# Kernel optimization log

Hardware: AMD Instinct MI355X
Metric: run time of the kernel (lower is better)

The kernel has to match this reference:

```python
import jax, jax.numpy as jnp
import numpy as np

B, T, S, D, H, DH = 2, 2048, 2048, 1024, 16, 64
LN_EPS = 1e-5


def setup_inputs() -> dict:
    key = jax.random.key(0)
    ks = jax.random.split(key, 8)
    return {
        "x": jax.random.normal(ks[0], (B, T, D), jnp.float32),
        "context": jax.random.normal(ks[1], (B, S, D), jnp.float32),
        "lookup_table": jax.random.normal(ks[2], (2 * T - 1, DH), jnp.float32),
        "Wq": jax.random.normal(ks[3], (D, H * DH), jnp.float32) * 0.02,
        "Wk": jax.random.normal(ks[4], (D, H * DH), jnp.float32) * 0.02,
        "Wv": jax.random.normal(ks[5], (D, H * DH), jnp.float32) * 0.02,
        "Wo": jax.random.normal(ks[6], (H * DH, D), jnp.float32) * 0.02,
        "bo": jnp.zeros((D,), jnp.float32),
        "gamma": jnp.ones((D,), jnp.float32),
        "beta": jnp.zeros((D,), jnp.float32),
    }


def skew(QE):
    # QE: [B, H, T, 2T-1] -> [B, H, T, T] via pad/reshape relative-position trick
    b, h, t, _ = QE.shape
    QE = jnp.pad(QE, ((0, 0), (0, 0), (0, 0), (0, 1))).reshape(b, h, -1)
    QE = jnp.pad(QE, ((0, 0), (0, 0), (0, t - 1))).reshape(b, h, t + 1, 2 * t - 1)
    return QE[:, :, :t, -t:]


def reference(x, context, lookup_table, Wq, Wk, Wv, Wo, bo, gamma, beta):
    scale = 1.0 / jnp.sqrt(jnp.asarray(DH, x.dtype))
    # pre-layernorm on queries
    mu = jnp.mean(x, axis=-1, keepdims=True)
    var = jnp.var(x, axis=-1, keepdims=True)
    xn = (x - mu) / jnp.sqrt(var + LN_EPS) * gamma + beta
    q = (xn @ Wq).reshape(B, T, H, DH).transpose(0, 2, 1, 3)       # [B,H,T,DH]
    k = (context @ Wk).reshape(B, S, H, DH).transpose(0, 2, 1, 3)  # [B,H,S,DH]
    v = (context @ Wv).reshape(B, S, H, DH).transpose(0, 2, 1, 3)  # [B,H,S,DH]
    score = jnp.einsum("bhtd,bhsd->bhts", q, k) * scale            # [B,H,T,S]
    rel = skew(jnp.einsum("bhtd,ld->bhtl", q, lookup_table))       # [B,H,T,T]
    # NOTE: faithful to original — QK^T gets scaled twice, rel term once
    score = (score + rel) * scale
    attn = jax.nn.softmax(score, axis=-1)
    out = jnp.einsum("bhts,bhsd->bhtd", attn, v)
    out = out.transpose(0, 2, 1, 3).reshape(B, T, H * DH)
    out = out @ Wo + bo
    # dropout=0 (eval); residual uses the layernormed x (as in source)
    return xn + out
```

## Files before the change

### kernel.cpp

```cpp
#include <hip/hip_runtime.h>

#define DEVFN __device__ __forceinline__

typedef __bf16 bf16x8 __attribute__((ext_vector_type(8)));
typedef float f32x4 __attribute__((ext_vector_type(4)));
typedef unsigned short u16;


DEVFN u16 f2bf(float f) {
  unsigned u = __builtin_bit_cast(unsigned, f);
  u += 0x7FFFu + ((u >> 16) & 1u);
  return (u16)(u >> 16);
}

DEVFN f32x4 mfma16(bf16x8 a, bf16x8 b, f32x4 c) {
  return __builtin_amdgcn_mfma_f32_16x16x32_bf16(a, b, c, 0, 0, 0);
}

DEVFN void gl16(const u16* g, u16* l) {
  __builtin_amdgcn_global_load_lds(
      (const __attribute__((address_space(1))) unsigned int*)g,
      (__attribute__((address_space(3))) unsigned int*)l, 16, 0, 0);
}

__global__ __launch_bounds__(256) void ln_kernel(const float* __restrict__ x,
                                                 const float* __restrict__ gamma,
                                                 const float* __restrict__ beta,
                                                 float* __restrict__ xn,
                                                 u16* __restrict__ xnb) {
  int row = blockIdx.x;
  int tid = threadIdx.x;
  const float4* xr = (const float4*)(x + (size_t)row * 1024);
  float4 v = xr[tid];
  float s = v.x + v.y + v.z + v.w;
  float q = v.x * v.x + v.y * v.y + v.z * v.z + v.w * v.w;
#pragma unroll
  for (int m = 1; m < 64; m <<= 1) {
    s += __shfl_xor(s, m);
    q += __shfl_xor(q, m);
  }
  __shared__ float rs[4], rq[4];
  int w = tid >> 6;
  if ((tid & 63) == 0) { rs[w] = s; rq[w] = q; }
  __syncthreads();
  s = rs[0] + rs[1] + rs[2] + rs[3];
  q = rq[0] + rq[1] + rq[2] + rq[3];
  float mean = s * (1.0f / 1024.0f);
  float var = q * (1.0f / 1024.0f) - mean * mean;
  float inv = rsqrtf(var + 1e-5f);
  float4 g = ((const float4*)gamma)[tid];
  float4 bt = ((const float4*)beta)[tid];
  float4 o;
  o.x = (v.x - mean) * inv * g.x + bt.x;
  o.y = (v.y - mean) * inv * g.y + bt.y;
  o.z = (v.z - mean) * inv * g.z + bt.z;
  o.w = (v.w - mean) * inv * g.w + bt.w;
  ((float4*)(xn + (size_t)row * 1024))[tid] = o;
  ushort4 ob;
  ob.x = f2bf(o.x); ob.y = f2bf(o.y); ob.z = f2bf(o.z); ob.w = f2bf(o.w);
  ((ushort4*)(xnb + (size_t)row * 1024))[tid] = ob;
}

__global__ __launch_bounds__(256) void cvt2_kernel(const float* __restrict__ a,
                                                   u16* __restrict__ oa,
                                                   const float* __restrict__ bsrc,
                                                   u16* __restrict__ ob) {
  int blk = blockIdx.x;
  if (blk < 4096) {
    int i = blk * 256 + threadIdx.x;
    float4 v = ((const float4*)a)[i];
    ushort4 o;
    o.x = f2bf(v.x); o.y = f2bf(v.y); o.z = f2bf(v.z); o.w = f2bf(v.w);
    ((ushort4*)oa)[i] = o;
  } else {
    int i = (blk - 4096) * 256 + threadIdx.x;
    if (i < 65520) {
      float4 v = ((const float4*)bsrc)[i];
      ushort4 o;
      o.x = f2bf(v.x); o.y = f2bf(v.y); o.z = f2bf(v.z); o.w = f2bf(v.w);
      ((ushort4*)ob)[i] = o;
    }
  }
}

__global__ __launch_bounds__(256) void transW_kernel(const float* __restrict__ W0,
                                                     const float* __restrict__ W1,
                                                     const float* __restrict__ W2,
                                                     const float* __restrict__ W3,
                                                     u16* __restrict__ Wall) {
  __shared__ float tile[32][33];
  int z = blockIdx.z;
  const float* W = (z == 0) ? W0 : (z == 1) ? W1 : (z == 2) ? W2 : W3;
  float scale = (z == 0) ? 0.18033688011112042f : (z == 1) ? 0.125f : 1.0f;
  u16* Wt = Wall + (size_t)z * 1048576;
  int tx = threadIdx.x, ty = threadIdx.y;
  int x = blockIdx.x * 32 + tx;
  int y0 = blockIdx.y * 32;
#pragma unroll
  for (int j = 0; j < 32; j += 8)
    tile[ty + j][tx] = W[(size_t)(y0 + ty + j) * 1024 + x];
  __syncthreads();
#pragma unroll
  for (int j = 0; j < 32; j += 8)
    Wt[(size_t)(blockIdx.x * 32 + ty + j) * 1024 + y0 + tx] = f2bf(tile[tx][ty + j] * scale);
}

DEVFN void gemm_core(const u16* __restrict__ A, const u16* __restrict__ Bt,
                     u16* Ab, u16* Bb, int row0, int n0, int tid,
                     f32x4 (&acc)[2][4]) {
  int lane = tid & 63, wv = tid >> 6;
  int l16 = lane & 15, lhi = lane >> 4;
  int r8 = lane >> 3, c8 = lane & 7;
  int cx = ((c8 ^ r8) << 3);
  int swz = (l16 & 7) << 3;

  auto stage = [&](int k0) {
#pragma unroll
    for (int i = 0; i < 4; ++i) {
      int rowb = wv * 32 + i * 8;
      gl16(&A[(size_t)(row0 + rowb + r8) * 1024 + k0 + cx], &Ab[rowb * 64]);
    }
#pragma unroll
    for (int i = 0; i < 2; ++i) {
      int rowb = wv * 16 + i * 8;
      gl16(&Bt[(size_t)(n0 + rowb + r8) * 1024 + k0 + cx], &Bb[rowb * 64]);
    }
  };

  stage(0);
  asm volatile("s_waitcnt vmcnt(0)" ::: "memory");
  __syncthreads();
  for (int kk = 0; kk < 16; ++kk) {
    __builtin_amdgcn_s_setprio(1);
#pragma unroll
    for (int ks = 0; ks < 2; ++ks) {
      bf16x8 af[2], bfr[4];
#pragma unroll
      for (int mi = 0; mi < 2; ++mi) {
        int row = wv * 32 + mi * 16 + l16;
        af[mi] = *(const bf16x8*)&Ab[row * 64 + ((ks * 32 + lhi * 8) ^ swz)];
      }
#pragma unroll
      for (int ni = 0; ni < 4; ++ni) {
        int row = ni * 16 + l16;
        bfr[ni] = *(const bf16x8*)&Bb[row * 64 + ((ks * 32 + lhi * 8) ^ swz)];
      }
#pragma unroll
      for (int mi = 0; mi < 2; ++mi)
#pragma unroll
        for (int ni = 0; ni < 4; ++ni)
          acc[mi][ni] = mfma16(af[mi], bfr[ni], acc[mi][ni]);
    }
    __builtin_amdgcn_s_setprio(0);
    if (kk < 15) {
      __syncthreads();
      stage((kk + 1) * 64);
      asm volatile("s_waitcnt vmcnt(0)" ::: "memory");
      __syncthreads();
    }
  }
}

__global__ __launch_bounds__(256, 4) void qkv_kernel(const u16* __restrict__ xnb,
                                                     const u16* __restrict__ ctxb,
                                                     const u16* __restrict__ Wall,
                                                     u16* __restrict__ qb,
                                                     u16* __restrict__ kb,
                                                     u16* __restrict__ vtb) {
  __shared__ __align__(16) u16 Ab[128 * 64];
  __shared__ __align__(16) u16 Bb[64 * 64];
  int z = blockIdx.z;
  const u16* A = (z == 0) ? xnb : ctxb;
  const u16* Bt = Wall + (size_t)z * 1048576;
  int row0 = blockIdx.x * 128, n0 = blockIdx.y * 64;
  f32x4 acc[2][4] = {};
  gemm_core(A, Bt, Ab, Bb, row0, n0, threadIdx.x, acc);
  int tid = threadIdx.x, lane = tid & 63, wv = tid >> 6;
  int l16 = lane & 15, lhi = lane >> 4;
  u16* qk = (z == 0) ? qb : kb;
#pragma unroll
  for (int mi = 0; mi < 2; ++mi)
#pragma unroll
    for (int ni = 0; ni < 4; ++ni)
#pragma unroll
      for (int r = 0; r < 4; ++r) {
        int m = row0 + wv * 32 + mi * 16 + lhi * 4 + r;
        int n = n0 + ni * 16 + l16;
        int b = m >> 11, t = m & 2047, h = n >> 6, dh = n & 63;
        u16 val = f2bf(acc[mi][ni][r]);
        if (z < 2) {
          qk[(size_t)((b * 16 + h) * 2048 + t) * 64 + dh] = val;
        } else {
          int t2 = (t & ~63) | ((t & 15) << 2) | ((t >> 4) & 3);
          vtb[(size_t)((b * 16 + h) * 64 + dh) * 2048 + t2] = val;
        }
      }
}

__global__ __launch_bounds__(256, 4) void oproj_kernel(const u16* __restrict__ attnb,
                                                       const u16* __restrict__ Wall,
                                                       const float* __restrict__ bias,
                                                       const float* __restrict__ resid,
                                                       float* __restrict__ outF) {
  __shared__ __align__(16) u16 Ab[128 * 64];
  __shared__ __align__(16) u16 Bb[64 * 64];
  const u16* Bt = Wall + (size_t)3 * 1048576;
  int row0 = blockIdx.x * 128, n0 = blockIdx.y * 64;
  f32x4 acc[2][4] = {};
  gemm_core(attnb, Bt, Ab, Bb, row0, n0, threadIdx.x, acc);
  int tid = threadIdx.x, lane = tid & 63, wv = tid >> 6;
  int l16 = lane & 15, lhi = lane >> 4;
#pragma unroll
  for (int mi = 0; mi < 2; ++mi)
#pragma unroll
    for (int ni = 0; ni < 4; ++ni)
#pragma unroll
      for (int r = 0; r < 4; ++r) {
        int m = row0 + wv * 32 + mi * 16 + lhi * 4 + r;
        int n = n0 + ni * 16 + l16;
        outF[(size_t)m * 1024 + n] = acc[mi][ni][r] + bias[n] + resid[(size_t)m * 1024 + n];
      }
}

__global__ __launch_bounds__(256, 4) void flash_kernel(
    const u16* __restrict__ Qg, const u16* __restrict__ Kg,
    const u16* __restrict__ Vtg, const u16* __restrict__ Lb,
    u16* __restrict__ Og) {
  constexpr int T = 2048, H = 16;
  int p = blockIdx.x;
  int bid = (p & 7) * 128 + (p >> 3);
  int qb = bid & 31, h = (bid >> 5) & 15, b = bid >> 9;
  int tid = threadIdx.x;
  int lane = tid & 63, w = tid >> 6;
  int l16 = lane & 15, lhi = lane >> 4;

  __shared__ __align__(16) u16 Klds[64 * 64];
  __shared__ __align__(16) u16 Vt[64 * 64];
  __shared__ __align__(16) u16 Llds[128 * 64];
  __shared__ __align__(16) u16 Plds[4][16 * 64];

  const u16* qbase = Qg + (size_t)(b * H + h) * T * 64;
  const u16* kbase = Kg + (size_t)(b * H + h) * T * 64;
  const u16* vtbase = Vtg + (size_t)(b * H + h) * 64 * 2048;

  int i0b = qb * 64;
  int i0w = i0b + w * 16;
  bf16x8 aq[2];
  aq[0] = *(const bf16x8*)&qbase[(i0w + l16) * 64 + lhi * 8];
  aq[1] = *(const bf16x8*)&qbase[(i0w + l16) * 64 + 32 + lhi * 8];

  f32x4 accO[4] = {};
  float mrun[4], lsum[4];
#pragma unroll
  for (int r = 0; r < 4; ++r) { mrun[r] = -1e30f; lsum[r] = 0.0f; }

  int bandbase = T - 16 - i0w;
  int ubase0 = T - 64 - i0b;
  int uoff = 48 - 16 * w;

  int r8 = lane >> 3, c8 = lane & 7;
  int cx = ((c8 ^ r8) << 3);
  int swz = (l16 & 7) << 3;

  auto stageKL = [&](int j0) {
#pragma unroll
    for (int i = 0; i < 2; ++i) {
      int rowb = w * 16 + i * 8;
      gl16(&kbase[(size_t)(j0 + rowb + r8) * 64 + cx], &Klds[rowb * 64]);
    }
#pragma unroll
    for (int i = 0; i < 4; ++i) {
      int rowb = w * 32 + i * 8;
      gl16(&Lb[(size_t)(ubase0 + j0 + rowb + r8) * 64 + cx], &Llds[rowb * 64]);
    }
  };
  auto stageV = [&](int j0) {
#pragma unroll
    for (int i = 0; i < 2; ++i) {
      int rowb = w * 16 + i * 8;
      gl16(&vtbase[(size_t)(rowb + r8) * 2048 + j0 + cx], &Vt[rowb * 64]);
    }
  };

  const u16* lp = Lb + (size_t)(bandbase + l16) * 64 + lhi * 8;
  f32x4 eC = {};
#pragma unroll
  for (int ks = 0; ks < 2; ++ks)
    eC = mfma16(aq[ks], *(const bf16x8*)&lp[ks * 32], eC);

  f32x4 accS[4];
  f32x4 accE[5];
  auto computeQKE = [&]() {
#pragma unroll
    for (int kb = 0; kb < 4; ++kb) accS[kb] = f32x4{0.f, 0.f, 0.f, 0.f};
    accE[0] = eC;
#pragma unroll
    for (int c = 1; c < 5; ++c) accE[c] = f32x4{0.f, 0.f, 0.f, 0.f};
    __builtin_amdgcn_s_setprio(1);
#pragma unroll
    for (int ks = 0; ks < 2; ++ks) {
#pragma unroll
      for (int kb = 0; kb < 4; ++kb) {
        int row = kb * 16 + l16;
        bf16x8 bk = *(const bf16x8*)&Klds[row * 64 + ((ks * 32 + lhi * 8) ^ swz)];
        accS[kb] = mfma16(aq[ks], bk, accS[kb]);
      }
#pragma unroll
      for (int c = 1; c < 5; ++c) {
        int urow = uoff + c * 16 + l16;
        bf16x8 bl = *(const bf16x8*)&Llds[urow * 64 + ((ks * 32 + lhi * 8) ^ swz)];
        accE[c] = mfma16(aq[ks], bl, accE[c]);
      }
    }
    __builtin_amdgcn_s_setprio(0);
    eC = accE[4];
  };

  const float THR = 11.541560327111707f;

  stageKL(0);
  asm volatile("s_waitcnt vmcnt(0)" ::: "memory");
  __syncthreads();
  stageV(0);
  computeQKE();

  for (int kt = 0; kt < 32; ++kt) {
    __syncthreads();
    if (kt < 31) stageKL((kt + 1) * 64);
    __builtin_amdgcn_sched_barrier(0);

    float sc[4][4];
    float lm[4];
    bool need = false;
#pragma unroll
    for (int r = 0; r < 4; ++r) {
      int m = lhi * 4 + r;
      int srcl = lhi * 16 + ((l16 - m + 15) & 15);
      bool lo = (l16 <= m);
      float e[5];
#pragma unroll
      for (int c = 0; c < 5; ++c) e[c] = __shfl(accE[c][r], srcl);
#pragma unroll
      for (int kb = 0; kb < 4; ++kb) sc[r][kb] = accS[kb][r] + (lo ? e[kb] : e[kb + 1]);
      lm[r] = fmaxf(fmaxf(sc[r][0], sc[r][1]), fmaxf(sc[r][2], sc[r][3]));
      need |= (lm[r] > mrun[r] + THR);
    }
    if (__ballot(need)) {
#pragma unroll
      for (int r = 0; r < 4; ++r) {
        float tm = lm[r];
        tm = fmaxf(tm, __shfl_xor(tm, 1));
        tm = fmaxf(tm, __shfl_xor(tm, 2));
        tm = fmaxf(tm, __shfl_xor(tm, 4));
        tm = fmaxf(tm, __shfl_xor(tm, 8));
        float mnew = fmaxf(mrun[r], tm);
        float al = exp2f(mrun[r] - mnew);
        mrun[r] = mnew;
        lsum[r] *= al;
#pragma unroll
        for (int dt = 0; dt < 4; ++dt) accO[dt][r] *= al;
      }
    }
#pragma unroll
    for (int r = 0; r < 4; ++r) {
      int m = lhi * 4 + r;
      float mm = mrun[r];
      float pv0 = exp2f(sc[r][0] - mm);
      float pv1 = exp2f(sc[r][1] - mm);
      float pv2 = exp2f(sc[r][2] - mm);
      float pv3 = exp2f(sc[r][3] - mm);
      lsum[r] += (pv0 + pv1) + (pv2 + pv3);
      unsigned pk01, pk23;
      asm("v_cvt_pk_bf16_f32 %0, %1, %2" : "=v"(pk01) : "v"(pv0), "v"(pv1));
      asm("v_cvt_pk_bf16_f32 %0, %1, %2" : "=v"(pk23) : "v"(pv2), "v"(pv3));
      uint2 pw;
      pw.x = pk01;
      pw.y = pk23;
      *(uint2*)&Plds[w][m * 64 + ((l16 * 4) ^ ((m & 7) << 3))] = pw;
    }

    __builtin_amdgcn_s_setprio(1);
#pragma unroll
    for (int ks = 0; ks < 2; ++ks) {
      bf16x8 ap = *(const bf16x8*)&Plds[w][l16 * 64 + ((ks * 32 + lhi * 8) ^ swz)];
#pragma unroll
      for (int dt = 0; dt < 4; ++dt) {
        int row = dt * 16 + l16;
        bf16x8 bv = *(const bf16x8*)&Vt[row * 64 + ((ks * 32 + lhi * 8) ^ swz)];
        accO[dt] = mfma16(ap, bv, accO[dt]);
      }
    }
    __builtin_amdgcn_s_setprio(0);

    __syncthreads();
    if (kt < 31) {
      stageV((kt + 1) * 64);
      __builtin_amdgcn_sched_barrier(0);
      computeQKE();
    }
  }

#pragma unroll
  for (int r = 0; r < 4; ++r) {
    float l = lsum[r];
    l += __shfl_xor(l, 1);
    l += __shfl_xor(l, 2);
    l += __shfl_xor(l, 4);
    l += __shfl_xor(l, 8);
    lsum[r] = 1.0f / l;
  }
#pragma unroll
  for (int dt = 0; dt < 4; ++dt)
#pragma unroll
    for (int r = 0; r < 4; ++r) {
      int i = i0w + lhi * 4 + r;
      int col = h * 64 + dt * 16 + l16;
      Og[(size_t)(b * T + i) * 1024 + col] = f2bf(accO[dt][r] * lsum[r]);
    }
}

extern "C" void kernel_launch(void* const* d_in, const int* in_sizes, int n_in,
                              void* d_out, int out_size, void* d_ws, size_t ws_size,
                              hipStream_t stream) {
  const float* x = (const float*)d_in[0];
  const float* ctx = (const float*)d_in[1];
  const float* Ltab = (const float*)d_in[2];
  const float* Wq = (const float*)d_in[3];
  const float* Wk = (const float*)d_in[4];
  const float* Wv = (const float*)d_in[5];
  const float* Wo = (const float*)d_in[6];
  const float* bo = (const float*)d_in[7];
  const float* gamma = (const float*)d_in[8];
  const float* beta = (const float*)d_in[9];
  float* out = (float*)d_out;

  size_t off = 0;
  auto take = [&](size_t bytes) {
    void* p = (char*)d_ws + off;
    off += (bytes + 255) & ~(size_t)255;
    return p;
  };
  u16* xnb = (u16*)take(8388608);
  u16* ctxb = (u16*)take(8388608);
  u16* Lb = (u16*)take(4095 * 64 * 2);
  u16* Wall = (u16*)take(4 * 2097152);
  u16* qbuf = (u16*)take(8388608);
  u16* kbuf = (u16*)take(8388608);
  u16* vtbuf = (u16*)take(8388608);
  u16* attnb = (u16*)take(8388608);

  ln_kernel<<<dim3(4096), dim3(256), 0, stream>>>(x, gamma, beta, out, xnb);
  cvt2_kernel<<<dim3(4096 + 256), dim3(256), 0, stream>>>(ctx, ctxb, Ltab, Lb);
  transW_kernel<<<dim3(32, 32, 4), dim3(32, 8), 0, stream>>>(Wq, Wk, Wv, Wo, Wall);
  qkv_kernel<<<dim3(32, 16, 3), dim3(256), 0, stream>>>(xnb, ctxb, Wall, qbuf, kbuf, vtbuf);
  flash_kernel<<<dim3(1024), dim3(256), 0, stream>>>(qbuf, kbuf, vtbuf, Lb, attnb);
  oproj_kernel<<<dim3(32, 16), dim3(256), 0, stream>>>(attnb, Wall, bo, out, out);
}
```

Before: 192.9 us.

## Process two 16-row query tiles per wave in flash attention kernel

Each wave now handles 32 query rows (two MFMA M-tiles) instead of 16, so each block covers 128 queries and the grid is halved to 512 blocks. K, V and relative-position table fragments loaded from LDS are reused across both tiles, which roughly halves LDS and global staging traffic per unit of work. The relative-band window grows to 192 rows and the carried band accumulators are adjusted to match. In exchange, register pressure rises, occupancy drops (launch bounds 4 to 2), and fewer blocks are available to fill the GPU.

```diff
diff --git a/kernel.cpp b/kernel.cpp
--- a/kernel.cpp
+++ b/kernel.cpp
@@ -222,41 +222,46 @@
       }
 }
 
-__global__ __launch_bounds__(256, 4) void flash_kernel(
+__global__ __launch_bounds__(256, 2) void flash_kernel(
     const u16* __restrict__ Qg, const u16* __restrict__ Kg,
     const u16* __restrict__ Vtg, const u16* __restrict__ Lb,
     u16* __restrict__ Og) {
   constexpr int T = 2048, H = 16;
   int p = blockIdx.x;
-  int bid = (p & 7) * 128 + (p >> 3);
-  int qb = bid & 31, h = (bid >> 5) & 15, b = bid >> 9;
+  int bid = (p & 7) * 64 + (p >> 3);
+  int qb = bid & 15, h = (bid >> 4) & 15, b = bid >> 8;
   int tid = threadIdx.x;
   int lane = tid & 63, w = tid >> 6;
   int l16 = lane & 15, lhi = lane >> 4;
 
   __shared__ __align__(16) u16 Klds[64 * 64];
   __shared__ __align__(16) u16 Vt[64 * 64];
-  __shared__ __align__(16) u16 Llds[128 * 64];
-  __shared__ __align__(16) u16 Plds[4][16 * 64];
+  __shared__ __align__(16) u16 Llds[192 * 64];
+  __shared__ __align__(16) u16 Plds[4][32 * 64];
 
   const u16* qbase = Qg + (size_t)(b * H + h) * T * 64;
   const u16* kbase = Kg + (size_t)(b * H + h) * T * 64;
   const u16* vtbase = Vtg + (size_t)(b * H + h) * 64 * 2048;
 
-  int i0b = qb * 64;
-  int i0w = i0b + w * 16;
-  bf16x8 aq[2];
-  aq[0] = *(const bf16x8*)&qbase[(i0w + l16) * 64 + lhi * 8];
-  aq[1] = *(const bf16x8*)&qbase[(i0w + l16) * 64 + 32 + lhi * 8];
-
-  f32x4 accO[4] = {};
-  float mrun[4], lsum[4];
-#pragma unroll
-  for (int r = 0; r < 4; ++r) { mrun[r] = -1e30f; lsum[r] = 0.0f; }
-
-  int bandbase = T - 16 - i0w;
-  int ubase0 = T - 64 - i0b;
-  int uoff = 48 - 16 * w;
+  int i0b = qb * 128;
+  int i0w = i0b + w * 32;
+  bf16x8 aq[2][2];
+#pragma unroll
+  for (int mt = 0; mt < 2; ++mt)
+#pragma unroll
+    for (int ks = 0; ks < 2; ++ks)
+      aq[mt][ks] = *(const bf16x8*)&qbase[(i0w + mt * 16 + l16) * 64 + ks * 32 + lhi * 8];
+
+  f32x4 accO[2][4] = {};
+  float mrun[2][4], lsum[2][4];
+#pragma unroll
+  for (int mt = 0; mt < 2; ++mt)
+#pragma unroll
+    for (int r = 0; r < 4; ++r) { mrun[mt][r] = -1e30f; lsum[mt][r] = 0.0f; }
+
+  int bstart0 = T - 32 - i0w;
+  int ubase0 = T - 128 - i0b;
+  int uoff = 96 - 32 * w;
 
   int r8 = lane >> 3, c8 = lane & 7;
   int cx = ((c8 ^ r8) << 3);
@@ -269,8 +274,8 @@
       gl16(&kbase[(size_t)(j0 + rowb + r8) * 64 + cx], &Klds[rowb * 64]);
     }
 #pragma unroll
-    for (int i = 0; i < 4; ++i) {
-      int rowb = w * 32 + i * 8;
+    for (int i = 0; i < 6; ++i) {
+      int rowb = w * 48 + i * 8;
       gl16(&Lb[(size_t)(ubase0 + j0 + rowb + r8) * 64 + cx], &Llds[rowb * 64]);
     }
   };
@@ -282,38 +287,49 @@
     }
   };
 
-  const u16* lp = Lb + (size_t)(bandbase + l16) * 64 + lhi * 8;
-  f32x4 eC = {};
+  f32x4 accE[2][6];
+#pragma unroll
+  for (int mt = 0; mt < 2; ++mt)
+#pragma unroll
+    for (int c = 0; c < 6; ++c) accE[mt][c] = f32x4{0.f, 0.f, 0.f, 0.f};
 #pragma unroll
   for (int ks = 0; ks < 2; ++ks)
-    eC = mfma16(aq[ks], *(const bf16x8*)&lp[ks * 32], eC);
-
-  f32x4 accS[4];
-  f32x4 accE[5];
+#pragma unroll
+    for (int c = 0; c < 2; ++c) {
+      bf16x8 bl = *(const bf16x8*)&Lb[(size_t)(bstart0 + c * 16 + l16) * 64 + ks * 32 + lhi * 8];
+      accE[0][4 + c] = mfma16(aq[0][ks], bl, accE[0][4 + c]);
+      accE[1][4 + c] = mfma16(aq[1][ks], bl, accE[1][4 + c]);
+    }
+
+  f32x4 accS[2][4];
   auto computeQKE = [&]() {
 #pragma unroll
-    for (int kb = 0; kb < 4; ++kb) accS[kb] = f32x4{0.f, 0.f, 0.f, 0.f};
-    accE[0] = eC;
-#pragma unroll
-    for (int c = 1; c < 5; ++c) accE[c] = f32x4{0.f, 0.f, 0.f, 0.f};
+    for (int mt = 0; mt < 2; ++mt) {
+#pragma unroll
+      for (int kb = 0; kb < 4; ++kb) accS[mt][kb] = f32x4{0.f, 0.f, 0.f, 0.f};
+      accE[mt][0] = accE[mt][4];
+      accE[mt][1] = accE[mt][5];
+#pragma unroll
+      for (int c = 2; c < 6; ++c) accE[mt][c] = f32x4{0.f, 0.f, 0.f, 0.f};
+    }
     __builtin_amdgcn_s_setprio(1);
 #pragma unroll
     for (int ks = 0; ks < 2; ++ks) {
 #pragma unroll
       for (int kb = 0; kb < 4; ++kb) {
-        int row = kb * 16 + l16;
-        bf16x8 bk = *(const bf16x8*)&Klds[row * 64 + ((ks * 32 + lhi * 8) ^ swz)];
-        accS[kb] = mfma16(aq[ks], bk, accS[kb]);
-      }
-#pragma unroll
-      for (int c = 1; c < 5; ++c) {
+        bf16x8 bk = *(const bf16x8*)&Klds[(kb * 16 + l16) * 64 + ((ks * 32 + lhi * 8) ^ swz)];
+        accS[0][kb] = mfma16(aq[0][ks], bk, accS[0][kb]);
+        accS[1][kb] = mfma16(aq[1][ks], bk, accS[1][kb]);
+      }
+#pragma unroll
+      for (int c = 2; c < 6; ++c) {
         int urow = uoff + c * 16 + l16;
         bf16x8 bl = *(const bf16x8*)&Llds[urow * 64 + ((ks * 32 + lhi * 8) ^ swz)];
-        accE[c] = mfma16(aq[ks], bl, accE[c]);
+        accE[0][c] = mfma16(aq[0][ks], bl, accE[0][c]);
+        accE[1][c] = mfma16(aq[1][ks], bl, accE[1][c]);
       }
     }
     __builtin_amdgcn_s_setprio(0);
-    eC = accE[4];
   };
 
   const float THR = 11.541560327111707f;
@@ -329,65 +345,79 @@
     if (kt < 31) stageKL((kt + 1) * 64);
     __builtin_amdgcn_sched_barrier(0);
 
-    float sc[4][4];
-    float lm[4];
+    float sc[2][4][4];
+    float lm[2][4];
     bool need = false;
 #pragma unroll
     for (int r = 0; r < 4; ++r) {
-      int m = lhi * 4 + r;
-      int srcl = lhi * 16 + ((l16 - m + 15) & 15);
-      bool lo = (l16 <= m);
-      float e[5];
-#pragma unroll
-      for (int c = 0; c < 5; ++c) e[c] = __shfl(accE[c][r], srcl);
-#pragma unroll
-      for (int kb = 0; kb < 4; ++kb) sc[r][kb] = accS[kb][r] + (lo ? e[kb] : e[kb + 1]);
-      lm[r] = fmaxf(fmaxf(sc[r][0], sc[r][1]), fmaxf(sc[r][2], sc[r][3]));
-      need |= (lm[r] > mrun[r] + THR);
+      int srcl = lhi * 16 + ((l16 - lhi * 4 - r + 15) & 15);
+      bool lo = (l16 <= lhi * 4 + r);
+      float e0[5], e1[5];
+#pragma unroll
+      for (int c = 0; c < 5; ++c) {
+        e0[c] = __shfl(accE[0][c + 1][r], srcl);
+        e1[c] = __shfl(accE[1][c][r], srcl);
+      }
+#pragma unroll
+      for (int kb = 0; kb < 4; ++kb) {
+        sc[0][r][kb] = accS[0][kb][r] + (lo ? e0[kb] : e0[kb + 1]);
+        sc[1][r][kb] = accS[1][kb][r] + (lo ? e1[kb] : e1[kb + 1]);
+      }
+#pragma unroll
+      for (int mt = 0; mt < 2; ++mt) {
+        lm[mt][r] = fmaxf(fmaxf(sc[mt][r][0], sc[mt][r][1]),
+                          fmaxf(sc[mt][r][2], sc[mt][r][3]));
+        need |= (lm[mt][r] > mrun[mt][r] + THR);
+      }
     }
     if (__ballot(need)) {
 #pragma unroll
-      for (int r = 0; r < 4; ++r) {
-        float tm = lm[r];
-        tm = fmaxf(tm, __shfl_xor(tm, 1));
-        tm = fmaxf(tm, __shfl_xor(tm, 2));
-        tm = fmaxf(tm, __shfl_xor(tm, 4));
-        tm = fmaxf(tm, __shfl_xor(tm, 8));
-        float mnew = fmaxf(mrun[r], tm);
-        float al = exp2f(mrun[r] - mnew);
-        mrun[r] = mnew;
-        lsum[r] *= al;
-#pragma unroll
-        for (int dt = 0; dt < 4; ++dt) accO[dt][r] *= al;
-      }
-    }
-#pragma unroll
-    for (int r = 0; r < 4; ++r) {
-      int m = lhi * 4 + r;
-      float mm = mrun[r];
-      float pv0 = exp2f(sc[r][0] - mm);
-      float pv1 = exp2f(sc[r][1] - mm);
-      float pv2 = exp2f(sc[r][2] - mm);
-      float pv3 = exp2f(sc[r][3] - mm);
-      lsum[r] += (pv0 + pv1) + (pv2 + pv3);
-      unsigned pk01, pk23;
-      asm("v_cvt_pk_bf16_f32 %0, %1, %2" : "=v"(pk01) : "v"(pv0), "v"(pv1));
-      asm("v_cvt_pk_bf16_f32 %0, %1, %2" : "=v"(pk23) : "v"(pv2), "v"(pv3));
-      uint2 pw;
-      pw.x = pk01;
-      pw.y = pk23;
-      *(uint2*)&Plds[w][m * 64 + ((l16 * 4) ^ ((m & 7) << 3))] = pw;
-    }
+      for (int mt = 0; mt < 2; ++mt)
+#pragma unroll
+        for (int r = 0; r < 4; ++r) {
+          float tm = lm[mt][r];
+          tm = fmaxf(tm, __shfl_xor(tm, 1));
+          tm = fmaxf(tm, __shfl_xor(tm, 2));
+          tm = fmaxf(tm, __shfl_xor(tm, 4));
+          tm = fmaxf(tm, __shfl_xor(tm, 8));
+          float mnew = fmaxf(mrun[mt][r], tm);
+          float al = exp2f(mrun[mt][r] - mnew);
+          mrun[mt][r] = mnew;
+          lsum[mt][r] *= al;
+#pragma unroll
+          for (int dt = 0; dt < 4; ++dt) accO[mt][dt][r] *= al;
+        }
+    }
+#pragma unroll
+    for (int r = 0; r < 4; ++r)
+#pragma unroll
+      for (int mt = 0; mt < 2; ++mt) {
+        int row = mt * 16 + lhi * 4 + r;
+        float mm = mrun[mt][r];
+        float pv0 = exp2f(sc[mt][r][0] - mm);
+        float pv1 = exp2f(sc[mt][r][1] - mm);
+        float pv2 = exp2f(sc[mt][r][2] - mm);
+        float pv3 = exp2f(sc[mt][r][3] - mm);
+        lsum[mt][r] += (pv0 + pv1) + (pv2 + pv3);
+        unsigned pk01, pk23;
+        asm("v_cvt_pk_bf16_f32 %0, %1, %2" : "=v"(pk01) : "v"(pv0), "v"(pv1));
+        asm("v_cvt_pk_bf16_f32 %0, %1, %2" : "=v"(pk23) : "v"(pv2), "v"(pv3));
+        uint2 pw;
+        pw.x = pk01;
+        pw.y = pk23;
+        *(uint2*)&Plds[w][row * 64 + ((l16 * 4) ^ ((row & 7) << 3))] = pw;
+      }
 
     __builtin_amdgcn_s_setprio(1);
 #pragma unroll
     for (int ks = 0; ks < 2; ++ks) {
-      bf16x8 ap = *(const bf16x8*)&Plds[w][l16 * 64 + ((ks * 32 + lhi * 8) ^ swz)];
+      bf16x8 ap0 = *(const bf16x8*)&Plds[w][(l16) * 64 + ((ks * 32 + lhi * 8) ^ swz)];
+      bf16x8 ap1 = *(const bf16x8*)&Plds[w][(16 + l16) * 64 + ((ks * 32 + lhi * 8) ^ swz)];
 #pragma unroll
       for (int dt = 0; dt < 4; ++dt) {
-        int row = dt * 16 + l16;
-        bf16x8 bv = *(const bf16x8*)&Vt[row * 64 + ((ks * 32 + lhi * 8) ^ swz)];
-        accO[dt] = mfma16(ap, bv, accO[dt]);
+        bf16x8 bv = *(const bf16x8*)&Vt[(dt * 16 + l16) * 64 + ((ks * 32 + lhi * 8) ^ swz)];
+        accO[0][dt] = mfma16(ap0, bv, accO[0][dt]);
+        accO[1][dt] = mfma16(ap1, bv, accO[1][dt]);
       }
     }
     __builtin_amdgcn_s_setprio(0);
@@ -401,22 +431,26 @@
   }
 
 #pragma unroll
-  for (int r = 0; r < 4; ++r) {
-    float l = lsum[r];
-    l += __shfl_xor(l, 1);
-    l += __shfl_xor(l, 2);
-    l += __shfl_xor(l, 4);
-    l += __shfl_xor(l, 8);
-    lsum[r] = 1.0f / l;
-  }
-#pragma unroll
-  for (int dt = 0; dt < 4; ++dt)
+  for (int mt = 0; mt < 2; ++mt)
 #pragma unroll
     for (int r = 0; r < 4; ++r) {
-      int i = i0w + lhi * 4 + r;
-      int col = h * 64 + dt * 16 + l16;
-      Og[(size_t)(b * T + i) * 1024 + col] = f2bf(accO[dt][r] * lsum[r]);
-    }
+      float l = lsum[mt][r];
+      l += __shfl_xor(l, 1);
+      l += __shfl_xor(l, 2);
+      l += __shfl_xor(l, 4);
+      l += __shfl_xor(l, 8);
+      lsum[mt][r] = 1.0f / l;
+    }
+#pragma unroll
+  for (int mt = 0; mt < 2; ++mt)
+#pragma unroll
+    for (int dt = 0; dt < 4; ++dt)
+#pragma unroll
+      for (int r = 0; r < 4; ++r) {
+        int i = i0w + mt * 16 + lhi * 4 + r;
+        int col = h * 64 + dt * 16 + l16;
+        Og[(size_t)(b * T + i) * 1024 + col] = f2bf(accO[mt][dt][r] * lsum[mt][r]);
+      }
 }
 
 extern "C" void kernel_launch(void* const* d_in, const int* in_sizes, int n_in,
@@ -453,6 +487,6 @@
   cvt2_kernel<<<dim3(4096 + 256), dim3(256), 0, stream>>>(ctx, ctxb, Ltab, Lb);
   transW_kernel<<<dim3(32, 32, 4), dim3(32, 8), 0, stream>>>(Wq, Wk, Wv, Wo, Wall);
   qkv_kernel<<<dim3(32, 16, 3), dim3(256), 0, stream>>>(xnb, ctxb, Wall, qbuf, kbuf, vtbuf);
-  flash_kernel<<<dim3(1024), dim3(256), 0, stream>>>(qbuf, kbuf, vtbuf, Lb, attnb);
+  flash_kernel<<<dim3(512), dim3(256), 0, stream>>>(qbuf, kbuf, vtbuf, Lb, attnb);
   oproj_kernel<<<dim3(32, 16), dim3(256), 0, stream>>>(attnb, Wall, bo, out, out);
 }
```

Measured after the change: 196.8 us. 1.02x slower.

## Reuse overlapping lookup-table rows in a ring buffer and pack shuffled rel-scores to bf16

Applied to the files above, without the earlier changes.

The lookup-table band for consecutive key tiles overlaps by 64 rows, so the LDS tile becomes a two-half ring buffer and only the 64 new rows are loaded each iteration instead of 128. Reads index the ring through a parity bit. Separately, four of the five cross-lane shuffles of relative-position scores are packed as bf16 pairs, halving those shuffles at the cost of rounding those terms to bf16 precision.

```diff
diff --git a/kernel.cpp b/kernel.cpp
--- a/kernel.cpp
+++ b/kernel.cpp
@@ -11,6 +11,10 @@
   unsigned u = __builtin_bit_cast(unsigned, f);
   u += 0x7FFFu + ((u >> 16) & 1u);
   return (u16)(u >> 16);
+}
+
+DEVFN float bfbits(unsigned hi) {
+  return __builtin_bit_cast(float, hi);
 }
 
 DEVFN f32x4 mfma16(bf16x8 a, bf16x8 b, f32x4 c) {
@@ -262,16 +266,19 @@
   int cx = ((c8 ^ r8) << 3);
   int swz = (l16 & 7) << 3;
 
-  auto stageKL = [&](int j0) {
+  auto stageK = [&](int j0) {
 #pragma unroll
     for (int i = 0; i < 2; ++i) {
       int rowb = w * 16 + i * 8;
       gl16(&kbase[(size_t)(j0 + rowb + r8) * 64 + cx], &Klds[rowb * 64]);
     }
-#pragma unroll
-    for (int i = 0; i < 4; ++i) {
-      int rowb = w * 32 + i * 8;
-      gl16(&Lb[(size_t)(ubase0 + j0 + rowb + r8) * 64 + cx], &Llds[rowb * 64]);
+  };
+  auto stageLnew = [&](int kt) {
+#pragma unroll
+    for (int i = 0; i < 2; ++i) {
+      int rowb = w * 16 + i * 8;
+      gl16(&Lb[(size_t)(ubase0 + kt * 64 + 128 + rowb + r8) * 64 + cx],
+           &Llds[((kt & 1) * 64 + rowb) * 64]);
     }
   };
   auto stageV = [&](int j0) {
@@ -290,7 +297,7 @@
 
   f32x4 accS[4];
   f32x4 accE[5];
-  auto computeQKE = [&]() {
+  auto computeQKE = [&](int tb) {
 #pragma unroll
     for (int kb = 0; kb < 4; ++kb) accS[kb] = f32x4{0.f, 0.f, 0.f, 0.f};
     accE[0] = eC;
@@ -307,8 +314,9 @@
       }
 #pragma unroll
       for (int c = 1; c < 5; ++c) {
-        int urow = uoff + c * 16 + l16;
-        bf16x8 bl = *(const bf16x8*)&Llds[urow * 64 + ((ks * 32 + lhi * 8) ^ swz)];
+        int ulog = uoff + c * 16;
+        int prow = ((((ulog >> 6) + tb) & 1) << 6) | ((ulog & 63) + l16);
+        bf16x8 bl = *(const bf16x8*)&Llds[prow * 64 + ((ks * 32 + lhi * 8) ^ swz)];
         accE[c] = mfma16(aq[ks], bl, accE[c]);
       }
     }
@@ -318,15 +326,23 @@
 
   const float THR = 11.541560327111707f;
 
-  stageKL(0);
+  stageK(0);
+#pragma unroll
+  for (int i = 0; i < 4; ++i) {
+    int rowb = w * 32 + i * 8;
+    gl16(&Lb[(size_t)(ubase0 + rowb + r8) * 64 + cx], &Llds[rowb * 64]);
+  }
   asm volatile("s_waitcnt vmcnt(0)" ::: "memory");
   __syncthreads();
   stageV(0);
-  computeQKE();
+  computeQKE(0);
 
   for (int kt = 0; kt < 32; ++kt) {
     __syncthreads();
-    if (kt < 31) stageKL((kt + 1) * 64);
+    if (kt < 31) {
+      stageK((kt + 1) * 64);
+      stageLnew(kt);
+    }
     __builtin_amdgcn_sched_barrier(0);
 
     float sc[4][4];
@@ -337,11 +353,18 @@
       int m = lhi * 4 + r;
       int srcl = lhi * 16 + ((l16 - m + 15) & 15);
       bool lo = (l16 <= m);
-      float e[5];
-#pragma unroll
-      for (int c = 0; c < 5; ++c) e[c] = __shfl(accE[c][r], srcl);
-#pragma unroll
-      for (int kb = 0; kb < 4; ++kb) sc[r][kb] = accS[kb][r] + (lo ? e[kb] : e[kb + 1]);
+      unsigned q01, q23;
+      asm("v_cvt_pk_bf16_f32 %0, %1, %2" : "=v"(q01) : "v"(accE[0][r]), "v"(accE[1][r]));
+      asm("v_cvt_pk_bf16_f32 %0, %1, %2" : "=v"(q23) : "v"(accE[2][r]), "v"(accE[3][r]));
+      q01 = (unsigned)__shfl((int)q01, srcl);
+      q23 = (unsigned)__shfl((int)q23, srcl);
+      float e4 = __shfl(accE[4][r], srcl);
+      float e0 = bfbits(q01 << 16), e1 = bfbits(q01 & 0xffff0000u);
+      float e2 = bfbits(q23 << 16), e3 = bfbits(q23 & 0xffff0000u);
+      sc[r][0] = accS[0][r] + (lo ? e0 : e1);
+      sc[r][1] = accS[1][r] + (lo ? e1 : e2);
+      sc[r][2] = accS[2][r] + (lo ? e2 : e3);
+      sc[r][3] = accS[3][r] + (lo ? e3 : e4);
       lm[r] = fmaxf(fmaxf(sc[r][0], sc[r][1]), fmaxf(sc[r][2], sc[r][3]));
       need |= (lm[r] > mrun[r] + THR);
     }
@@ -396,7 +419,7 @@
     if (kt < 31) {
       stageV((kt + 1) * 64);
       __builtin_amdgcn_sched_barrier(0);
-      computeQKE();
+      computeQKE((kt + 1) & 1);
     }
   }
 
```

Measured after the change: 190.9 us (median of 2 runs). Within noise of the previous version (-1.0%).
